# Optimization experiments

Measured on AMD Instinct MI355X. Metric: run time of the kernel, lower is better.

The kernel has to match this reference:

```python
import jax, jax.numpy as jnp
import numpy as np

WP = 1.0     # warp_penalty
TEMP = 0.01  # soft-min temperature
BIG = 1e7    # finite stand-in for +inf (exp(-BIG/TEMP) == 0 exactly in fp32)


def setup_inputs() -> dict:
    key = jax.random.key(0)
    k1, k2, k3, k4 = jax.random.split(key, 4)
    B, T1, T2, C = 8, 256, 1024, 128
    fea_a = jax.random.normal(k1, (B, T1, C), jnp.float32)
    fea_b = jax.random.normal(k2, (B, T2, C), jnp.float32)
    len_a = jax.random.randint(k3, (B,), T1 // 2, T1 + 1)
    len_b = jax.random.randint(k4, (B,), T2 // 2, T2 + 1)
    return {"fea_a": fea_a, "len_a": len_a, "fea_b": fea_b, "len_b": len_b}


def _softmin(v, temp):
    # v: [3, B, T1]; stable -temp*log(sum(exp(-v/temp)))
    m = jnp.min(v, axis=0)
    return m - temp * jnp.log(jnp.sum(jnp.exp(-(v - m) / temp), axis=0))


def _soft_dtw(fea_a, fea_b, len_a, len_b, wp=WP, temp=TEMP):
    B, T1, C = fea_a.shape
    T2 = fea_b.shape[1]
    # L1 cost: [B, T2, T1]  (rows index fea_b, cols index fea_a, as in torch code)
    cost = jnp.mean(jnp.abs(fea_a[:, None, :, :] - fea_b[:, :, None, :]), axis=-1)
    # skewed cost: skew[b, d, j] = cost[b, clip(d-j, 0, T2-1), j]
    D = T1 + T2 - 1
    d = jnp.arange(D)[:, None]
    j = jnp.arange(T1)[None, :]
    idx = jnp.clip(d - j, 0, T2 - 1)           # [D, T1]
    skew = cost[:, idx, j]                      # [B, D, T1]
    skew = jnp.swapaxes(skew, 0, 1)             # [D, B, T1] for scan

    pc0 = jnp.full((B, T1 + 1), BIG, jnp.float32)       # path_cost (diag d-1)
    pcp0 = pc0.at[:, 0].set(0.0)                         # path_cost_prev (diag d-2)

    def step(carry, crow):
        pc, pcp = carry
        dirs = jnp.stack([pcp[:, :-1], pc[:, 1:] + wp, pc[:, :-1] + wp], axis=0)
        new = crow + _softmin(dirs, temp)                # [B, T1]
        new = jnp.concatenate([jnp.full((B, 1), BIG, new.dtype), new], axis=1)
        return (new, pc), new

    _, ys = jax.lax.scan(step, (pc0, pcp0), skew)        # ys: [D, B, T1+1]
    # per-sample answer: diagonal len_a+len_b-2, entry len_a
    di = len_a + len_b - 2
    loss_i = ys[di, jnp.arange(B), len_a]
    return jnp.sum(loss_i)  # reduction='mean' over a length-1 accumulator == sum


def reference(fea_a, len_a, fea_b, len_b):
    return _soft_dtw(fea_a, fea_b, len_a, len_b)
```

## Files before the change

### kernel.cpp

```cpp
#include <hip/hip_runtime.h>
#include <hip/hip_bf16.h>
#include <hip/hip_fp16.h>
#include <cstddef>
#include <cstdint>

#define BIGV 10000000.0f
#define WPV  1.0f

#define BATCH 8
#define T1N 256
#define T2N 1024
#define CN 128
#define DN 1279

#define FLAG_MAGIC 0x600D0000

typedef __attribute__((ext_vector_type(2))) _Float16 half2v;

__global__ __launch_bounds__(256) void cost_kernel(const float* __restrict__ A,
                                                   const float* __restrict__ Bf,
                                                   const int* __restrict__ lenA,
                                                   const int* __restrict__ lenB,
                                                   float* __restrict__ sk) {
    __shared__ char As[64 * 256];
    __shared__ char Bs[95 * 256];

    const int b  = blockIdx.z;
    const int d0 = blockIdx.y * 32;
    const int j0 = blockIdx.x * 64;
    const int tid = threadIdx.x;

    const int dEnd = lenA[b] + lenB[b] - 2;
    if (d0 > dEnd) return;

    const float* Ab = A  + (size_t)b * T1N * CN;
    const float* Bb = Bf + (size_t)b * T2N * CN;

    const int tj = tid & 15;
    const int td = tid >> 4;
    const int brow0 = td - tj + 63;
    const int rbase = d0 - j0 - 63;

#define SWB(row, g) (((row) << 8) + ((((g) + (row)) & 15) << 4))

    #pragma unroll
    for (int i = 0; i < 8; ++i) {
        int idx = tid + i * 256;
        int row = idx >> 5;
        int q   = idx & 31;
        float4 f = *(const float4*)(Ab + (size_t)(j0 + row) * CN + (q << 2));
        half2v h0 = { (_Float16)f.x, (_Float16)f.y };
        half2v h1 = { (_Float16)f.z, (_Float16)f.w };
        char* dst = As + SWB(row, q >> 1) + ((q & 1) << 3);
        ((uint32_t*)dst)[0] = __builtin_bit_cast(uint32_t, h0);
        ((uint32_t*)dst)[1] = __builtin_bit_cast(uint32_t, h1);
    }
    #pragma unroll
    for (int i = 0; i < 12; ++i) {
        int idx = tid + i * 256;
        if (idx < 3040) {
            int row = idx >> 5;
            int q   = idx & 31;
            int gr = rbase + row;
            gr = gr < 0 ? 0 : (gr > T2N - 1 ? T2N - 1 : gr);
            float4 f = *(const float4*)(Bb + (size_t)gr * CN + (q << 2));
            half2v h0 = { (_Float16)f.x, (_Float16)f.y };
            half2v h1 = { (_Float16)f.z, (_Float16)f.w };
            char* dst = Bs + SWB(row, q >> 1) + ((q & 1) << 3);
            ((uint32_t*)dst)[0] = __builtin_bit_cast(uint32_t, h0);
            ((uint32_t*)dst)[1] = __builtin_bit_cast(uint32_t, h1);
        }
    }
    __syncthreads();

    float acc[2][4];
    #pragma unroll
    for (int i = 0; i < 2; ++i)
        #pragma unroll
        for (int j = 0; j < 4; ++j) acc[i][j] = 0.0f;

    const half2v one2 = { (_Float16)1.0f, (_Float16)1.0f };

    for (int g = 0; g < 16; ++g) {
        uint4 a4[4], bv[5];
        #pragma unroll
        for (int ji = 0; ji < 4; ++ji) {
            int row = tj + 16 * ji;
            a4[ji] = *(const uint4*)(As + SWB(row, g));
        }
        #pragma unroll
        for (int m = 0; m < 5; ++m) {
            int row = brow0 + 16 * (m - 3);
            bv[m] = *(const uint4*)(Bs + SWB(row, g));
        }
        #pragma unroll
        for (int dk = 0; dk < 2; ++dk) {
            #pragma unroll
            for (int ji = 0; ji < 4; ++ji) {
                uint4 au = a4[ji];
                uint4 bu = bv[dk - ji + 3];
                float a = acc[dk][ji];
                #pragma unroll
                for (int w = 0; w < 4; ++w) {
                    uint32_t ua = (&au.x)[w];
                    uint32_t ub = (&bu.x)[w];
                    half2v d2 = __builtin_bit_cast(half2v, ua)
                              - __builtin_bit_cast(half2v, ub);
                    uint32_t du = __builtin_bit_cast(uint32_t, d2) & 0x7FFF7FFFu;
#if __has_builtin(__builtin_amdgcn_fdot2)
                    a = __builtin_amdgcn_fdot2(__builtin_bit_cast(half2v, du),
                                               one2, a, false);
#else
                    half2v ad = __builtin_bit_cast(half2v, du);
                    a += (float)ad.x + (float)ad.y;
#endif
                }
                acc[dk][ji] = a;
            }
        }
    }
#undef SWB

    #pragma unroll
    for (int dk = 0; dk < 2; ++dk) {
        int d = d0 + td + 16 * dk;
        if (d < DN) {
            size_t rowoff = ((size_t)b * DN + d) * T1N;
            #pragma unroll
            for (int ji = 0; ji < 4; ++ji) {
                int j = j0 + tj + 16 * ji;
                sk[rowoff + j] = acc[dk][ji] * (1.0f / 128.0f);
            }
        }
    }
}

__device__ __forceinline__ float min3f(float a, float b, float c) {
    float d;
    asm("v_min3_f32 %0, %1, %2, %3" : "=v"(d) : "v"(a), "v"(b), "v"(c));
    return d;
}

__global__ __launch_bounds__(64, 1) void dp_reg_kernel(const float* __restrict__ sk,
                                                       const int* __restrict__ lenA,
                                                       const int* __restrict__ lenB,
                                                       float* __restrict__ partials,
                                                       int* __restrict__ flags,
                                                       float* __restrict__ out) {
    const int b = blockIdx.x;
    const int L = threadIdx.x;

    const int la = __builtin_amdgcn_readfirstlane(lenA[b]);
    const int lb = __builtin_amdgcn_readfirstlane(lenB[b]);
    const int dEnd = la + lb - 2;
    const int kLast = dEnd >> 4;

    const char* lanep = (const char*)(sk + (size_t)b * DN * T1N) + (L << 4);

    float v1_0 = BIGV, v1_1 = BIGV, v1_2 = BIGV, v1_3 = BIGV;
    float v2_0 = BIGV, v2_1 = BIGV, v2_2 = BIGV, v2_3 = BIGV;
    float p1_prev = (L == 0) ? 0.0f : BIGV;

    float4 A0, A1, A2, A3, A4, A5, A6, A7, A8, A9, A10, A11, A12, A13, A14, A15;
    float4 B0, B1, B2, B3, B4, B5, B6, B7, B8, B9, B10, B11, B12, B13, B14, B15;

#define SHFL_UP1(SRC)                                                       \
    __int_as_float(__builtin_amdgcn_update_dpp(                             \
        __float_as_int(BIGV), __float_as_int(SRC),                          \
        0x138 , 0xF, 0xF, false))

#define LOAD1(DST, KB, R) do {                                              \
        int row_ = ((KB) << 4) + (R);                                       \
        row_ = row_ > dEnd ? dEnd : row_;                                   \
        DST = *(const float4*)(lanep + (size_t)row_ * (T1N * 4));           \
    } while (0)

#define LOADALL(P, KB) do {                                                 \
        LOAD1(P##0, KB, 0);   LOAD1(P##1, KB, 1);   LOAD1(P##2, KB, 2);     \
        LOAD1(P##3, KB, 3);   LOAD1(P##4, KB, 4);   LOAD1(P##5, KB, 5);     \
        LOAD1(P##6, KB, 6);   LOAD1(P##7, KB, 7);   LOAD1(P##8, KB, 8);     \
        LOAD1(P##9, KB, 9);   LOAD1(P##10, KB, 10); LOAD1(P##11, KB, 11);   \
        LOAD1(P##12, KB, 12); LOAD1(P##13, KB, 13); LOAD1(P##14, KB, 14);   \
        LOAD1(P##15, KB, 15);                                               \
    } while (0)

#define DP_STEP(C4) do {                                                    \
        float4 c = (C4);                                                    \
        float p1 = SHFL_UP1(v1_3);                                          \
        float w0 = v1_0 + WPV, w1 = v1_1 + WPV;                             \
        float w2 = v1_2 + WPV, w3 = v1_3 + WPV;                             \
        float wp = p1 + WPV;                                                \
        float n0 = c.x + min3f(p1_prev, w0, wp);                            \
        float n1 = c.y + min3f(v2_0, w1, w0);                               \
        float n2 = c.z + min3f(v2_1, w2, w1);                               \
        float n3 = c.w + min3f(v2_2, w3, w2);                               \
        p1_prev = p1;                                                       \
        v2_0 = v1_0; v2_1 = v1_1; v2_2 = v1_2; v2_3 = v1_3;                 \
        v1_0 = n0;   v1_1 = n1;   v1_2 = n2;   v1_3 = n3;                   \
    } while (0)

#define DP_STEP_G(C4, R) do {                                               \
        float4 c = (C4);                                                    \
        float p1 = SHFL_UP1(v1_3);                                          \
        float w0 = v1_0 + WPV, w1 = v1_1 + WPV;                             \
        float w2 = v1_2 + WPV, w3 = v1_3 + WPV;                             \
        float wp = p1 + WPV;                                                \
        float n0 = c.x + min3f(p1_prev, w0, wp);                            \
        float n1 = c.y + min3f(v2_0, w1, w0);                               \
        float n2 = c.z + min3f(v2_1, w2, w1);                               \
        float n3 = c.w + min3f(v2_2, w3, w2);                               \
        if ((R) <= rem) {                                                   \
            p1_prev = p1;                                                   \
            v2_0 = v1_0; v2_1 = v1_1; v2_2 = v1_2; v2_3 = v1_3;             \
            v1_0 = n0;   v1_1 = n1;   v1_2 = n2;   v1_3 = n3;               \
        }                                                                   \
    } while (0)

#define STEP_RL(C4, KB, R) do { DP_STEP(C4); LOAD1(C4, KB, R); } while (0)

#define PROC_RELOAD(P, KB) do {                                             \
        STEP_RL(P##0, KB, 0);   STEP_RL(P##1, KB, 1);                       \
        STEP_RL(P##2, KB, 2);   STEP_RL(P##3, KB, 3);                       \
        STEP_RL(P##4, KB, 4);   STEP_RL(P##5, KB, 5);                       \
        STEP_RL(P##6, KB, 6);   STEP_RL(P##7, KB, 7);                       \
        STEP_RL(P##8, KB, 8);   STEP_RL(P##9, KB, 9);                       \
        STEP_RL(P##10, KB, 10); STEP_RL(P##11, KB, 11);                     \
        STEP_RL(P##12, KB, 12); STEP_RL(P##13, KB, 13);                     \
        STEP_RL(P##14, KB, 14); STEP_RL(P##15, KB, 15);                     \
    } while (0)

#define PROC_FULL(P) do {                                                   \
        DP_STEP(P##0);  DP_STEP(P##1);  DP_STEP(P##2);  DP_STEP(P##3);      \
        DP_STEP(P##4);  DP_STEP(P##5);  DP_STEP(P##6);  DP_STEP(P##7);      \
        DP_STEP(P##8);  DP_STEP(P##9);  DP_STEP(P##10); DP_STEP(P##11);     \
        DP_STEP(P##12); DP_STEP(P##13); DP_STEP(P##14); DP_STEP(P##15);     \
    } while (0)

#define PROC_GUARD(P) do {                                                  \
        DP_STEP_G(P##0, 0);   DP_STEP_G(P##1, 1);   DP_STEP_G(P##2, 2);     \
        DP_STEP_G(P##3, 3);   DP_STEP_G(P##4, 4);   DP_STEP_G(P##5, 5);     \
        DP_STEP_G(P##6, 6);   DP_STEP_G(P##7, 7);   DP_STEP_G(P##8, 8);     \
        DP_STEP_G(P##9, 9);   DP_STEP_G(P##10, 10); DP_STEP_G(P##11, 11);   \
        DP_STEP_G(P##12, 12); DP_STEP_G(P##13, 13); DP_STEP_G(P##14, 14);   \
        DP_STEP_G(P##15, 15);                                               \
    } while (0)

    LOADALL(A, 0);
    LOADALL(B, 1);

    int k = 0;
    while (k + 1 < kLast) {
        PROC_RELOAD(A, k + 2);
        PROC_RELOAD(B, k + 3);
        k += 2;
    }
    if (k < kLast) {
        PROC_FULL(A);
        const int rem = dEnd & 15;
        PROC_GUARD(B);
    } else {
        const int rem = dEnd & 15;
        PROC_GUARD(A);
    }

    const int tcap = la - 1;
    if (L == (tcap >> 2)) {
        const int kk = tcap & 3;
        float r = v1_0;
        if (kk == 1) r = v1_1;
        else if (kk == 2) r = v1_2;
        else if (kk == 3) r = v1_3;
        partials[b] = r;
        __threadfence();
        __hip_atomic_store(&flags[b], FLAG_MAGIC + b,
                           __ATOMIC_RELEASE, __HIP_MEMORY_SCOPE_AGENT);
    }

    if (b == 0 && L == 0) {
        float s = 0.0f;
        for (int i = 0; i < BATCH; ++i) {
            while (__hip_atomic_load(&flags[i], __ATOMIC_ACQUIRE,
                                     __HIP_MEMORY_SCOPE_AGENT) != FLAG_MAGIC + i)
                __builtin_amdgcn_s_sleep(2);
            s += __hip_atomic_load(&partials[i], __ATOMIC_RELAXED,
                                   __HIP_MEMORY_SCOPE_AGENT);
        }
        out[0] = s;
    }
#undef PROC_GUARD
#undef PROC_FULL
#undef PROC_RELOAD
#undef STEP_RL
#undef DP_STEP_G
#undef DP_STEP
#undef LOADALL
#undef LOAD1
#undef SHFL_UP1
}

extern "C" void kernel_launch(void* const* d_in, const int* in_sizes, int n_in,
                              void* d_out, int out_size, void* d_ws, size_t ws_size,
                              hipStream_t stream) {
    const float* feaA = (const float*)d_in[0];
    const int*   lenA = (const int*)d_in[1];
    const float* feaB = (const float*)d_in[2];
    const int*   lenB = (const int*)d_in[3];

    float* sk = (float*)d_ws;
    float* partials = (float*)((char*)d_ws + (size_t)BATCH * DN * T1N * sizeof(float));
    int*   flags    = (int*)(partials + BATCH);

    cost_kernel<<<dim3(T1N / 64, (DN + 31) / 32, BATCH), 256, 0, stream>>>(feaA, feaB, lenA, lenB, sk);
    dp_reg_kernel<<<BATCH, 64, 0, stream>>>(sk, lenA, lenB, partials, flags, (float*)d_out);
}
```

Measured before the change: 135.4 us.

## Interleave two length-sorted batch DP chains per wavefront in a dual kernel

The DP kernel now launches 4 wavefronts instead of 8. Each wavefront sorts the batch items by diagonal length and runs two neighbouring items' anti-diagonal recurrences interleaved step by step, then finishes the longer one alone. The aim is to fill the latency bubbles of each serial min3/DPP dependency chain with independent work from a second chain. The cost is a doubled per-wave instruction and load stream and fewer active CUs, so the critical path may lengthen if the single chain was not purely latency-bound.

```diff
diff --git a/kernel.cpp b/kernel.cpp
--- a/kernel.cpp
+++ b/kernel.cpp
@@ -141,142 +141,185 @@
     return d;
 }
 
-__global__ __launch_bounds__(64, 1) void dp_reg_kernel(const float* __restrict__ sk,
-                                                       const int* __restrict__ lenA,
-                                                       const int* __restrict__ lenB,
-                                                       float* __restrict__ partials,
-                                                       int* __restrict__ flags,
-                                                       float* __restrict__ out) {
-    const int b = blockIdx.x;
+__global__ __launch_bounds__(64, 1) void dp_dual_kernel(const float* __restrict__ sk,
+                                                        const int* __restrict__ lenA,
+                                                        const int* __restrict__ lenB,
+                                                        float* __restrict__ partials,
+                                                        int* __restrict__ flags,
+                                                        float* __restrict__ out) {
+    const int blk = blockIdx.x;
     const int L = threadIdx.x;
 
-    const int la = __builtin_amdgcn_readfirstlane(lenA[b]);
-    const int lb = __builtin_amdgcn_readfirstlane(lenB[b]);
-    const int dEnd = la + lb - 2;
-    const int kLast = dEnd >> 4;
-
-    const char* lanep = (const char*)(sk + (size_t)b * DN * T1N) + (L << 4);
-
-    float v1_0 = BIGV, v1_1 = BIGV, v1_2 = BIGV, v1_3 = BIGV;
-    float v2_0 = BIGV, v2_1 = BIGV, v2_2 = BIGV, v2_3 = BIGV;
-    float p1_prev = (L == 0) ? 0.0f : BIGV;
-
-    float4 A0, A1, A2, A3, A4, A5, A6, A7, A8, A9, A10, A11, A12, A13, A14, A15;
-    float4 B0, B1, B2, B3, B4, B5, B6, B7, B8, B9, B10, B11, B12, B13, B14, B15;
+    int ds[8], is[8];
+    for (int i = 0; i < 8; ++i) { ds[i] = lenA[i] + lenB[i] - 2; is[i] = i; }
+    for (int i = 1; i < 8; ++i) {
+        int dv = ds[i], iv = is[i];
+        int j = i - 1;
+        while (j >= 0 && ds[j] > dv) { ds[j+1] = ds[j]; is[j+1] = is[j]; --j; }
+        ds[j+1] = dv; is[j+1] = iv;
+    }
+    const int bA    = __builtin_amdgcn_readfirstlane(is[2*blk]);
+    const int bB    = __builtin_amdgcn_readfirstlane(is[2*blk+1]);
+    const int dEndA = __builtin_amdgcn_readfirstlane(ds[2*blk]);
+    const int dEndB = __builtin_amdgcn_readfirstlane(ds[2*blk+1]);
+    const int laA   = __builtin_amdgcn_readfirstlane(lenA[bA]);
+    const int laB   = __builtin_amdgcn_readfirstlane(lenB ? lenA[bB] : 0);
+    const int kLastA = dEndA >> 4;
+    const int kLastB = dEndB >> 4;
+
+    const char* lanepA = (const char*)(sk + (size_t)bA * DN * T1N) + (L << 4);
+    const char* lanepB = (const char*)(sk + (size_t)bB * DN * T1N) + (L << 4);
+
+    float v1a_0 = BIGV, v1a_1 = BIGV, v1a_2 = BIGV, v1a_3 = BIGV;
+    float v2a_0 = BIGV, v2a_1 = BIGV, v2a_2 = BIGV, v2a_3 = BIGV;
+    float v1b_0 = BIGV, v1b_1 = BIGV, v1b_2 = BIGV, v1b_3 = BIGV;
+    float v2b_0 = BIGV, v2b_1 = BIGV, v2b_2 = BIGV, v2b_3 = BIGV;
+    float ppa = (L == 0) ? 0.0f : BIGV;
+    float ppb = (L == 0) ? 0.0f : BIGV;
+
+    float4 CA0, CA1, CA2, CA3, CA4, CA5, CA6, CA7,
+           CA8, CA9, CA10, CA11, CA12, CA13, CA14, CA15;
+    float4 CB0, CB1, CB2, CB3, CB4, CB5, CB6, CB7,
+           CB8, CB9, CB10, CB11, CB12, CB13, CB14, CB15;
 
 #define SHFL_UP1(SRC)                                                       \
     __int_as_float(__builtin_amdgcn_update_dpp(                             \
         __float_as_int(BIGV), __float_as_int(SRC),                          \
         0x138 , 0xF, 0xF, false))
 
-#define LOAD1(DST, KB, R) do {                                              \
+#define LOAD1X(DST, PFX, KB, R) do {                                        \
         int row_ = ((KB) << 4) + (R);                                       \
-        row_ = row_ > dEnd ? dEnd : row_;                                   \
-        DST = *(const float4*)(lanep + (size_t)row_ * (T1N * 4));           \
-    } while (0)
-
-#define LOADALL(P, KB) do {                                                 \
-        LOAD1(P##0, KB, 0);   LOAD1(P##1, KB, 1);   LOAD1(P##2, KB, 2);     \
-        LOAD1(P##3, KB, 3);   LOAD1(P##4, KB, 4);   LOAD1(P##5, KB, 5);     \
-        LOAD1(P##6, KB, 6);   LOAD1(P##7, KB, 7);   LOAD1(P##8, KB, 8);     \
-        LOAD1(P##9, KB, 9);   LOAD1(P##10, KB, 10); LOAD1(P##11, KB, 11);   \
-        LOAD1(P##12, KB, 12); LOAD1(P##13, KB, 13); LOAD1(P##14, KB, 14);   \
-        LOAD1(P##15, KB, 15);                                               \
-    } while (0)
-
-#define DP_STEP(C4) do {                                                    \
-        float4 c = (C4);                                                    \
-        float p1 = SHFL_UP1(v1_3);                                          \
-        float w0 = v1_0 + WPV, w1 = v1_1 + WPV;                             \
-        float w2 = v1_2 + WPV, w3 = v1_3 + WPV;                             \
-        float wp = p1 + WPV;                                                \
-        float n0 = c.x + min3f(p1_prev, w0, wp);                            \
-        float n1 = c.y + min3f(v2_0, w1, w0);                               \
-        float n2 = c.z + min3f(v2_1, w2, w1);                               \
-        float n3 = c.w + min3f(v2_2, w3, w2);                               \
-        p1_prev = p1;                                                       \
-        v2_0 = v1_0; v2_1 = v1_1; v2_2 = v1_2; v2_3 = v1_3;                 \
-        v1_0 = n0;   v1_1 = n1;   v1_2 = n2;   v1_3 = n3;                   \
-    } while (0)
-
-#define DP_STEP_G(C4, R) do {                                               \
-        float4 c = (C4);                                                    \
-        float p1 = SHFL_UP1(v1_3);                                          \
-        float w0 = v1_0 + WPV, w1 = v1_1 + WPV;                             \
-        float w2 = v1_2 + WPV, w3 = v1_3 + WPV;                             \
-        float wp = p1 + WPV;                                                \
-        float n0 = c.x + min3f(p1_prev, w0, wp);                            \
-        float n1 = c.y + min3f(v2_0, w1, w0);                               \
-        float n2 = c.z + min3f(v2_1, w2, w1);                               \
-        float n3 = c.w + min3f(v2_2, w3, w2);                               \
-        if ((R) <= rem) {                                                   \
-            p1_prev = p1;                                                   \
-            v2_0 = v1_0; v2_1 = v1_1; v2_2 = v1_2; v2_3 = v1_3;             \
-            v1_0 = n0;   v1_1 = n1;   v1_2 = n2;   v1_3 = n3;               \
+        row_ = row_ > dEnd##PFX ? dEnd##PFX : row_;                         \
+        DST = *(const float4*)(lanep##PFX + (size_t)row_ * (T1N * 4));      \
+    } while (0)
+
+#define DP_STEPX(C4, P) do {                                                \
+        float4 c_ = (C4);                                                   \
+        float p1_ = SHFL_UP1(v1##P##_3);                                    \
+        float w0_ = v1##P##_0 + WPV, w1_ = v1##P##_1 + WPV;                 \
+        float w2_ = v1##P##_2 + WPV, w3_ = v1##P##_3 + WPV;                 \
+        float wp_ = p1_ + WPV;                                              \
+        float n0_ = c_.x + min3f(pp##P, w0_, wp_);                          \
+        float n1_ = c_.y + min3f(v2##P##_0, w1_, w0_);                      \
+        float n2_ = c_.z + min3f(v2##P##_1, w2_, w1_);                      \
+        float n3_ = c_.w + min3f(v2##P##_2, w3_, w2_);                      \
+        pp##P = p1_;                                                        \
+        v2##P##_0 = v1##P##_0; v2##P##_1 = v1##P##_1;                       \
+        v2##P##_2 = v1##P##_2; v2##P##_3 = v1##P##_3;                       \
+        v1##P##_0 = n0_; v1##P##_1 = n1_; v1##P##_2 = n2_; v1##P##_3 = n3_; \
+    } while (0)
+
+#define DP_STEPX_G(C4, P, R, REM) do {                                      \
+        float4 c_ = (C4);                                                   \
+        float p1_ = SHFL_UP1(v1##P##_3);                                    \
+        float w0_ = v1##P##_0 + WPV, w1_ = v1##P##_1 + WPV;                 \
+        float w2_ = v1##P##_2 + WPV, w3_ = v1##P##_3 + WPV;                 \
+        float wp_ = p1_ + WPV;                                              \
+        float n0_ = c_.x + min3f(pp##P, w0_, wp_);                          \
+        float n1_ = c_.y + min3f(v2##P##_0, w1_, w0_);                      \
+        float n2_ = c_.z + min3f(v2##P##_1, w2_, w1_);                      \
+        float n3_ = c_.w + min3f(v2##P##_2, w3_, w2_);                      \
+        if ((R) <= (REM)) {                                                 \
+            pp##P = p1_;                                                    \
+            v2##P##_0 = v1##P##_0; v2##P##_1 = v1##P##_1;                   \
+            v2##P##_2 = v1##P##_2; v2##P##_3 = v1##P##_3;                   \
+            v1##P##_0 = n0_; v1##P##_1 = n1_;                               \
+            v1##P##_2 = n2_; v1##P##_3 = n3_;                               \
         }                                                                   \
     } while (0)
 
-#define STEP_RL(C4, KB, R) do { DP_STEP(C4); LOAD1(C4, KB, R); } while (0)
-
-#define PROC_RELOAD(P, KB) do {                                             \
-        STEP_RL(P##0, KB, 0);   STEP_RL(P##1, KB, 1);                       \
-        STEP_RL(P##2, KB, 2);   STEP_RL(P##3, KB, 3);                       \
-        STEP_RL(P##4, KB, 4);   STEP_RL(P##5, KB, 5);                       \
-        STEP_RL(P##6, KB, 6);   STEP_RL(P##7, KB, 7);                       \
-        STEP_RL(P##8, KB, 8);   STEP_RL(P##9, KB, 9);                       \
-        STEP_RL(P##10, KB, 10); STEP_RL(P##11, KB, 11);                     \
-        STEP_RL(P##12, KB, 12); STEP_RL(P##13, KB, 13);                     \
-        STEP_RL(P##14, KB, 14); STEP_RL(P##15, KB, 15);                     \
-    } while (0)
-
-#define PROC_FULL(P) do {                                                   \
-        DP_STEP(P##0);  DP_STEP(P##1);  DP_STEP(P##2);  DP_STEP(P##3);      \
-        DP_STEP(P##4);  DP_STEP(P##5);  DP_STEP(P##6);  DP_STEP(P##7);      \
-        DP_STEP(P##8);  DP_STEP(P##9);  DP_STEP(P##10); DP_STEP(P##11);     \
-        DP_STEP(P##12); DP_STEP(P##13); DP_STEP(P##14); DP_STEP(P##15);     \
-    } while (0)
-
-#define PROC_GUARD(P) do {                                                  \
-        DP_STEP_G(P##0, 0);   DP_STEP_G(P##1, 1);   DP_STEP_G(P##2, 2);     \
-        DP_STEP_G(P##3, 3);   DP_STEP_G(P##4, 4);   DP_STEP_G(P##5, 5);     \
-        DP_STEP_G(P##6, 6);   DP_STEP_G(P##7, 7);   DP_STEP_G(P##8, 8);     \
-        DP_STEP_G(P##9, 9);   DP_STEP_G(P##10, 10); DP_STEP_G(P##11, 11);   \
-        DP_STEP_G(P##12, 12); DP_STEP_G(P##13, 13); DP_STEP_G(P##14, 14);   \
-        DP_STEP_G(P##15, 15);                                               \
-    } while (0)
-
-    LOADALL(A, 0);
-    LOADALL(B, 1);
-
-    int k = 0;
-    while (k + 1 < kLast) {
-        PROC_RELOAD(A, k + 2);
-        PROC_RELOAD(B, k + 3);
-        k += 2;
-    }
-    if (k < kLast) {
-        PROC_FULL(A);
-        const int rem = dEnd & 15;
-        PROC_GUARD(B);
-    } else {
-        const int rem = dEnd & 15;
-        PROC_GUARD(A);
-    }
-
-    const int tcap = la - 1;
-    if (L == (tcap >> 2)) {
-        const int kk = tcap & 3;
-        float r = v1_0;
-        if (kk == 1) r = v1_1;
-        else if (kk == 2) r = v1_2;
-        else if (kk == 3) r = v1_3;
-        partials[b] = r;
-        __threadfence();
-        __hip_atomic_store(&flags[b], FLAG_MAGIC + b,
-                           __ATOMIC_RELEASE, __HIP_MEMORY_SCOPE_AGENT);
-    }
-
-    if (b == 0 && L == 0) {
+#define DROW(R) do {                                                        \
+        DP_STEPX(CA##R, a); LOAD1X(CA##R, A, k + 1, R);                     \
+        DP_STEPX(CB##R, b); LOAD1X(CB##R, B, k + 1, R);                     \
+    } while (0)
+
+#define BROW(R) do {                                                        \
+        DP_STEPX(CB##R, b); LOAD1X(CB##R, B, k2 + 1, R);                    \
+    } while (0)
+
+    LOAD1X(CA0, A, 0, 0);   LOAD1X(CB0, B, 0, 0);
+    LOAD1X(CA1, A, 0, 1);   LOAD1X(CB1, B, 0, 1);
+    LOAD1X(CA2, A, 0, 2);   LOAD1X(CB2, B, 0, 2);
+    LOAD1X(CA3, A, 0, 3);   LOAD1X(CB3, B, 0, 3);
+    LOAD1X(CA4, A, 0, 4);   LOAD1X(CB4, B, 0, 4);
+    LOAD1X(CA5, A, 0, 5);   LOAD1X(CB5, B, 0, 5);
+    LOAD1X(CA6, A, 0, 6);   LOAD1X(CB6, B, 0, 6);
+    LOAD1X(CA7, A, 0, 7);   LOAD1X(CB7, B, 0, 7);
+    LOAD1X(CA8, A, 0, 8);   LOAD1X(CB8, B, 0, 8);
+    LOAD1X(CA9, A, 0, 9);   LOAD1X(CB9, B, 0, 9);
+    LOAD1X(CA10, A, 0, 10); LOAD1X(CB10, B, 0, 10);
+    LOAD1X(CA11, A, 0, 11); LOAD1X(CB11, B, 0, 11);
+    LOAD1X(CA12, A, 0, 12); LOAD1X(CB12, B, 0, 12);
+    LOAD1X(CA13, A, 0, 13); LOAD1X(CB13, B, 0, 13);
+    LOAD1X(CA14, A, 0, 14); LOAD1X(CB14, B, 0, 14);
+    LOAD1X(CA15, A, 0, 15); LOAD1X(CB15, B, 0, 15);
+
+    for (int k = 0; k < kLastA; ++k) {
+        DROW(0);  DROW(1);  DROW(2);  DROW(3);
+        DROW(4);  DROW(5);  DROW(6);  DROW(7);
+        DROW(8);  DROW(9);  DROW(10); DROW(11);
+        DROW(12); DROW(13); DROW(14); DROW(15);
+    }
+
+    {
+        const int remA = dEndA & 15;
+        DP_STEPX_G(CA0, a, 0, remA);   DP_STEPX_G(CA1, a, 1, remA);
+        DP_STEPX_G(CA2, a, 2, remA);   DP_STEPX_G(CA3, a, 3, remA);
+        DP_STEPX_G(CA4, a, 4, remA);   DP_STEPX_G(CA5, a, 5, remA);
+        DP_STEPX_G(CA6, a, 6, remA);   DP_STEPX_G(CA7, a, 7, remA);
+        DP_STEPX_G(CA8, a, 8, remA);   DP_STEPX_G(CA9, a, 9, remA);
+        DP_STEPX_G(CA10, a, 10, remA); DP_STEPX_G(CA11, a, 11, remA);
+        DP_STEPX_G(CA12, a, 12, remA); DP_STEPX_G(CA13, a, 13, remA);
+        DP_STEPX_G(CA14, a, 14, remA); DP_STEPX_G(CA15, a, 15, remA);
+    }
+    {
+        const int tcap = laA - 1;
+        if (L == (tcap >> 2)) {
+            const int kk = tcap & 3;
+            float r = v1a_0;
+            if (kk == 1) r = v1a_1;
+            else if (kk == 2) r = v1a_2;
+            else if (kk == 3) r = v1a_3;
+            partials[bA] = r;
+            __threadfence();
+            __hip_atomic_store(&flags[bA], FLAG_MAGIC + bA,
+                               __ATOMIC_RELEASE, __HIP_MEMORY_SCOPE_AGENT);
+        }
+    }
+
+    for (int k2 = kLastA; k2 < kLastB; ++k2) {
+        BROW(0);  BROW(1);  BROW(2);  BROW(3);
+        BROW(4);  BROW(5);  BROW(6);  BROW(7);
+        BROW(8);  BROW(9);  BROW(10); BROW(11);
+        BROW(12); BROW(13); BROW(14); BROW(15);
+    }
+    {
+        const int remB = dEndB & 15;
+        DP_STEPX_G(CB0, b, 0, remB);   DP_STEPX_G(CB1, b, 1, remB);
+        DP_STEPX_G(CB2, b, 2, remB);   DP_STEPX_G(CB3, b, 3, remB);
+        DP_STEPX_G(CB4, b, 4, remB);   DP_STEPX_G(CB5, b, 5, remB);
+        DP_STEPX_G(CB6, b, 6, remB);   DP_STEPX_G(CB7, b, 7, remB);
+        DP_STEPX_G(CB8, b, 8, remB);   DP_STEPX_G(CB9, b, 9, remB);
+        DP_STEPX_G(CB10, b, 10, remB); DP_STEPX_G(CB11, b, 11, remB);
+        DP_STEPX_G(CB12, b, 12, remB); DP_STEPX_G(CB13, b, 13, remB);
+        DP_STEPX_G(CB14, b, 14, remB); DP_STEPX_G(CB15, b, 15, remB);
+    }
+    {
+        const int tcap = laB - 1;
+        if (L == (tcap >> 2)) {
+            const int kk = tcap & 3;
+            float r = v1b_0;
+            if (kk == 1) r = v1b_1;
+            else if (kk == 2) r = v1b_2;
+            else if (kk == 3) r = v1b_3;
+            partials[bB] = r;
+            __threadfence();
+            __hip_atomic_store(&flags[bB], FLAG_MAGIC + bB,
+                               __ATOMIC_RELEASE, __HIP_MEMORY_SCOPE_AGENT);
+        }
+    }
+
+    if (blk == 0 && L == 0) {
         float s = 0.0f;
         for (int i = 0; i < BATCH; ++i) {
             while (__hip_atomic_load(&flags[i], __ATOMIC_ACQUIRE,
@@ -287,14 +330,11 @@
         }
         out[0] = s;
     }
-#undef PROC_GUARD
-#undef PROC_FULL
-#undef PROC_RELOAD
-#undef STEP_RL
-#undef DP_STEP_G
-#undef DP_STEP
-#undef LOADALL
-#undef LOAD1
+#undef BROW
+#undef DROW
+#undef DP_STEPX_G
+#undef DP_STEPX
+#undef LOAD1X
 #undef SHFL_UP1
 }
 
@@ -311,5 +351,5 @@
     int*   flags    = (int*)(partials + BATCH);
 
     cost_kernel<<<dim3(T1N / 64, (DN + 31) / 32, BATCH), 256, 0, stream>>>(feaA, feaB, lenA, lenB, sk);
-    dp_reg_kernel<<<BATCH, 64, 0, stream>>>(sk, lenA, lenB, partials, flags, (float*)d_out);
+    dp_dual_kernel<<<4, 64, 0, stream>>>(sk, lenA, lenB, partials, flags, (float*)d_out);
 }
```

Measured after the change: 183.5 us. +35.5%, slower.
